# Kernel tuning notes

Hardware: AMD Instinct MI355X
Metric: run time of the kernel (lower is better)

Reference implementation:

```python
import jax, jax.numpy as jnp
import numpy as np

N_POINTS = 8192
N_TOPICS = 64
B = 524288


def setup_inputs() -> dict:
    key = jax.random.key(0)
    k1, k2, k3, k4 = jax.random.split(key, 4)
    pij = jax.random.uniform(k1, (B,), dtype=jnp.float32, minval=1e-6, maxval=1.0)
    i = jax.random.randint(k2, (B,), 0, N_POINTS, dtype=jnp.int64)
    j = jax.random.randint(k3, (B,), 0, N_POINTS, dtype=jnp.int64)
    W = jax.random.normal(k4, (N_POINTS, N_TOPICS), dtype=jnp.float32)  # nn.Embedding weight
    return {"pij": pij, "i": i, "j": j, "W": W}


def reference(pij, i, j, W):
    # pairwise squared distances over ALL points, via the gram trick
    # (avoids materializing the [n, n, d] broadcasted tensor of the torch code)
    sq = jnp.sum(W * W, axis=1)                       # [n]
    d2 = sq[:, None] + sq[None, :] - 2.0 * (W @ W.T)  # [n, n]
    d2 = jnp.maximum(d2, 0.0)                         # numerical floor (exact math is >= 0)
    n = W.shape[0]
    # Cauchy kernel partition: sum_{k,l} 1/(1+d2) minus the n diagonal ones
    part = jnp.sum(1.0 / (1.0 + d2)) - jnp.asarray(n, d2.dtype)
    xi = W[i]                                         # [B, d]
    xj = W[j]                                         # [B, d]
    # FAITHFUL to source: (1 + diff^2).sum(1) adds 1 per dim => n_topics + ||xi-xj||^2
    num = 1.0 / jnp.sum(1.0 + (xi - xj) ** 2, axis=1)  # [B]
    qij = num / part
    loss_kld = pij * (jnp.log(pij) - jnp.log(qij))
    return jnp.sum(loss_kld)
```

## Files before the change

### kernel.cpp

```cpp
#include <hip/hip_runtime.h>
#include <math.h>

#define NPOINTS   8192
#define NDIM      64
#define TILE      128
#define NT2       64
#define NBLK      2080
#define NGRP      512

#define WS_W16   0
#define WS_W8    262144
#define WS_SQ    393216
#define WS_PARTA 401408
#define WS_A1P   403488
#define WS_A3P   407584

typedef __attribute__((ext_vector_type(8))) short bf16x8;
typedef __attribute__((ext_vector_type(4))) float f32x4;
typedef __attribute__((ext_vector_type(2))) float f32x2;

__device__ inline unsigned f2bf_pk(float lo, float hi) {
    unsigned ul = __float_as_uint(lo), uh = __float_as_uint(hi);
    ul += 0x7FFFu + ((ul >> 16) & 1u);
    uh += 0x7FFFu + ((uh >> 16) & 1u);
    return (ul >> 16) | (uh & 0xFFFF0000u);
}
template <bool HI>
__device__ inline f32x2 cvt2(unsigned dw) {
    return __builtin_amdgcn_cvt_pk_f32_fp8((int)dw, HI);
}
__device__ inline void sqacc(f32x2& s, unsigned a, unsigned b) {
    f32x2 dl = cvt2<false>(a) - cvt2<false>(b);
    f32x2 dh = cvt2<true >(a) - cvt2<true >(b);
    s += dl * dl;
    s += dh * dh;
}

__global__ __launch_bounds__(256) void prep_kernel(const float* __restrict__ W,
                                                   float* __restrict__ sq,
                                                   unsigned* __restrict__ W16f,
                                                   unsigned* __restrict__ W8) {
    int g = blockIdx.x;
    int t = threadIdx.x;

    {
        int h = t >> 7, L = (t >> 1) & 63, dp = t & 1;
        int row = g * 16 + (L & 15), quad = L >> 4;
        float4 v = *(const float4*)(W + row * NDIM + h * 32 + quad * 8 + dp * 4);
        uint2 o;
        o.x = f2bf_pk(v.x, v.y);
        o.y = f2bf_pk(v.z, v.w);
        *(uint2*)(W16f + ((g * 2 + h) * 256 + L * 4 + dp * 2)) = o;
    }
    {
        int r = t >> 4, s = t & 15;
        float4 v = *(const float4*)(W + (g * 16 + r) * NDIM + s * 4);
        float p = v.x * v.x + v.y * v.y + v.z * v.z + v.w * v.w;
        p += __shfl_xor(p, 1, 64);
        p += __shfl_xor(p, 2, 64);
        p += __shfl_xor(p, 4, 64);
        p += __shfl_xor(p, 8, 64);
        if (s == 0) sq[g * 16 + r] = p;
    }
    {
        int r = g * 16 + (t >> 4), d = t & 15;
        float4 x = *(const float4*)(W + r * NDIM + d * 4);
        int lo = __builtin_amdgcn_cvt_pk_fp8_f32(x.x, x.y, 0, false);
        int dw = __builtin_amdgcn_cvt_pk_fp8_f32(x.z, x.w, lo, true);
        W8[r * 16 + d] = (unsigned)dw;
    }
}

__global__ __launch_bounds__(256) void pair_kernel(const unsigned* __restrict__ W8,
                                                   const float* __restrict__ pij,
                                                   const int* __restrict__ ii,
                                                   const int* __restrict__ jj,
                                                   int nb,
                                                   float* __restrict__ a1p,
                                                   float* __restrict__ a3p) {
    int t = threadIdx.x;
    int p = blockIdx.x * 256 + t;
    float a1 = 0.f, a3 = 0.f;
    if (p < nb) {
        int   i  = ii[p];
        int   j  = jj[p];
        float pv = pij[p];
        const uint4* X = (const uint4*)(W8 + i * 16);
        const uint4* Y = (const uint4*)(W8 + j * 16);
        uint4 x0 = X[0], x1 = X[1], x2 = X[2], x3 = X[3];
        uint4 y0 = Y[0], y1 = Y[1], y2 = Y[2], y3 = Y[3];
        f32x2 s2 = {0.f, 0.f};
        sqacc(s2, x0.x, y0.x); sqacc(s2, x0.y, y0.y);
        sqacc(s2, x0.z, y0.z); sqacc(s2, x0.w, y0.w);
        sqacc(s2, x1.x, y1.x); sqacc(s2, x1.y, y1.y);
        sqacc(s2, x1.z, y1.z); sqacc(s2, x1.w, y1.w);
        sqacc(s2, x2.x, y2.x); sqacc(s2, x2.y, y2.y);
        sqacc(s2, x2.z, y2.z); sqacc(s2, x2.w, y2.w);
        sqacc(s2, x3.x, y3.x); sqacc(s2, x3.y, y3.y);
        sqacc(s2, x3.z, y3.z); sqacc(s2, x3.w, y3.w);
        float v = s2.x + s2.y;
        a1 = pv * __logf(pv * ((float)NDIM + v));
        a3 = pv;
    }
    #pragma unroll
    for (int m = 32; m >= 1; m >>= 1) {
        a1 += __shfl_xor(a1, m, 64);
        a3 += __shfl_xor(a3, m, 64);
    }
    __shared__ float red[8];
    if ((t & 63) == 0) { red[t >> 6] = a1; red[4 + (t >> 6)] = a3; }
    __syncthreads();
    if (t == 0) {
        a1p[blockIdx.x] = red[0] + red[1] + red[2] + red[3];
        a3p[blockIdx.x] = red[4] + red[5] + red[6] + red[7];
    }
}

__global__ __launch_bounds__(256) void pairwise_kernel(const unsigned* __restrict__ W16f,
                                                       const float* __restrict__ sq,
                                                       float* __restrict__ partA) {
    int z = blockIdx.x;
    int t = threadIdx.x, w = t >> 6, lane = t & 63;
    int by = (int)((129.0f - sqrtf((float)(16641 - 8 * z))) * 0.5f);
    while (by * NT2 - by * (by - 1) / 2 > z) --by;
    while ((by + 1) * NT2 - (by + 1) * by / 2 <= z) ++by;
    int bx = by + (z - (by * NT2 - by * (by - 1) / 2));

    int wm = w >> 1, wn = w & 1, quad = lane >> 4, l15 = lane & 15;
    int a0 = by * TILE, b0 = bx * TILE;

    float4 base1[4];
    float  sqb[4];
    {
        int arow = a0 + wm * 64 + quad * 4;
        #pragma unroll
        for (int tm = 0; tm < 4; ++tm) {
            float4 v = *(const float4*)(sq + arow + tm * 16);
            base1[tm] = (float4){1.0f + v.x, 1.0f + v.y, 1.0f + v.z, 1.0f + v.w};
        }
        int bcol = b0 + wn * 64 + l15;
        #pragma unroll
        for (int tn = 0; tn < 4; ++tn) sqb[tn] = sq[bcol + tn * 16];
    }

    f32x4 acc[4][4];
    #pragma unroll
    for (int i = 0; i < 4; ++i)
        #pragma unroll
        for (int j = 0; j < 4; ++j) acc[i][j] = (f32x4){0.f, 0.f, 0.f, 0.f};

    int gA = (a0 >> 4) + wm * 4;
    int gB = (b0 >> 4) + wn * 4;
    #pragma unroll
    for (int h = 0; h < 2; ++h) {
        bf16x8 af[4], bfr[4];
        #pragma unroll
        for (int tm = 0; tm < 4; ++tm)
            af[tm] = *(const bf16x8*)(W16f + (((gA + tm) * 2 + h) * 256 + lane * 4));
        #pragma unroll
        for (int tn = 0; tn < 4; ++tn)
            bfr[tn] = *(const bf16x8*)(W16f + (((gB + tn) * 2 + h) * 256 + lane * 4));
        #pragma unroll
        for (int tm = 0; tm < 4; ++tm)
            #pragma unroll
            for (int tn = 0; tn < 4; ++tn)
                acc[tm][tn] = __builtin_amdgcn_mfma_f32_16x16x32_bf16(af[tm], bfr[tn],
                                                                      acc[tm][tn], 0, 0, 0);
    }

    float ssum = 0.f;
    if (bx > by) {
        #pragma unroll
        for (int tn = 0; tn < 4; ++tn) {
            float c0 = sqb[tn];
            #pragma unroll
            for (int tm = 0; tm < 4; ++tm) {
                ssum += __builtin_amdgcn_rcpf(fmaf(acc[tm][tn][0], -2.0f, base1[tm].x + c0));
                ssum += __builtin_amdgcn_rcpf(fmaf(acc[tm][tn][1], -2.0f, base1[tm].y + c0));
                ssum += __builtin_amdgcn_rcpf(fmaf(acc[tm][tn][2], -2.0f, base1[tm].z + c0));
                ssum += __builtin_amdgcn_rcpf(fmaf(acc[tm][tn][3], -2.0f, base1[tm].w + c0));
            }
        }
    } else {
        int quad4 = quad * 4;
        #pragma unroll
        for (int tn = 0; tn < 4; ++tn) {
            int cl = wn * 64 + tn * 16 + l15;
            float c0 = sqb[tn];
            float b4[4];
            #pragma unroll
            for (int tm = 0; tm < 4; ++tm) {
                b4[0] = base1[tm].x; b4[1] = base1[tm].y;
                b4[2] = base1[tm].z; b4[3] = base1[tm].w;
                #pragma unroll
                for (int r = 0; r < 4; ++r) {
                    int rl = wm * 64 + tm * 16 + quad4 + r;
                    float inv = __builtin_amdgcn_rcpf(fmaf(acc[tm][tn][r], -2.0f, b4[r] + c0));
                    ssum += (cl > rl) ? inv : 0.f;
                }
            }
        }
    }
    #pragma unroll
    for (int m = 32; m >= 1; m >>= 1) ssum += __shfl_xor(ssum, m, 64);
    __shared__ float wsum[4];
    if (lane == 0) wsum[w] = ssum;
    __syncthreads();
    if (t == 0) partA[z] = wsum[0] + wsum[1] + wsum[2] + wsum[3];
}

__global__ __launch_bounds__(256) void final_kernel(const float* __restrict__ partA,
                                                    const float* __restrict__ a1p,
                                                    const float* __restrict__ a3p,
                                                    int npb,
                                                    float* __restrict__ out) {
    __shared__ double r1[256], r2[256], r3[256];
    int t = threadIdx.x;
    double dpart = 0.0, d1 = 0.0, d3 = 0.0;
    for (int k = t; k < NBLK; k += 256) dpart += (double)partA[k];
    for (int k = t; k < npb; k += 256) { d1 += (double)a1p[k]; d3 += (double)a3p[k]; }
    r1[t] = dpart; r2[t] = d1; r3[t] = d3;
    __syncthreads();
    for (int s = 128; s >= 1; s >>= 1) {
        if (t < s) { r1[t] += r1[t + s]; r2[t] += r2[t + s]; r3[t] += r3[t + s]; }
        __syncthreads();
    }
    if (t == 0) {
        double part = 2.0 * r1[0];
        out[0] = (float)(r2[0] + r3[0] * log(part));
    }
}

extern "C" void kernel_launch(void* const* d_in, const int* in_sizes, int n_in,
                              void* d_out, int out_size, void* d_ws, size_t ws_size,
                              hipStream_t stream) {
    const float* pij = (const float*)d_in[0];
    const int*   ii  = (const int*)d_in[1];
    const int*   jj  = (const int*)d_in[2];
    const float* W   = (const float*)d_in[3];
    float* out = (float*)d_out;
    float* ws  = (float*)d_ws;

    unsigned* W16f  = (unsigned*)ws + WS_W16;
    unsigned* W8    = (unsigned*)ws + WS_W8;
    float*    sqv   = ws + WS_SQ;
    float*    partA = ws + WS_PARTA;
    float*    a1p   = ws + WS_A1P;
    float*    a3p   = ws + WS_A3P;

    int nb  = in_sizes[0];
    int npb = (nb + 255) / 256;

    prep_kernel<<<NGRP, 256, 0, stream>>>(W, sqv, W16f, W8);
    pair_kernel<<<npb, 256, 0, stream>>>(W8, pij, ii, jj, nb, a1p, a3p);
    pairwise_kernel<<<NBLK, 256, 0, stream>>>(W16f, sqv, partA);
    final_kernel<<<1, 256, 0, stream>>>(partA, a1p, a3p, npb, out);
}
```

Baseline: 91.37 us.

## Merge pair, pairwise and final kernels into one launch with last-block reduction

Fuses the pair-loss kernel, the pairwise Cauchy partition kernel and the final reduction into a single grid, where blocks are split by index between the two workloads. The last block to finish, found with an atomic counter, does the final double-precision reduction. The pair path now uses 4 lanes per pair with 16-byte loads and a shuffle reduction. This removes two kernel launches and lets the two independent stages overlap, at the cost of a threadfence and an atomic per block and 4x more pair blocks.

Result: slower. 285.8 us (+212.8%).

```diff
diff --git a/kernel.cpp b/kernel.cpp
--- a/kernel.cpp
+++ b/kernel.cpp
@@ -13,7 +13,8 @@
 #define WS_SQ    393216
 #define WS_PARTA 401408
 #define WS_A1P   403488
-#define WS_A3P   407584
+#define WS_A3P   411680
+#define WS_CNT   419872
 
 typedef __attribute__((ext_vector_type(8))) short bf16x8;
 typedef __attribute__((ext_vector_type(4))) float f32x4;
@@ -39,9 +40,11 @@
 __global__ __launch_bounds__(256) void prep_kernel(const float* __restrict__ W,
                                                    float* __restrict__ sq,
                                                    unsigned* __restrict__ W16f,
-                                                   unsigned* __restrict__ W8) {
+                                                   unsigned* __restrict__ W8,
+                                                   unsigned* __restrict__ cnt) {
     int g = blockIdx.x;
     int t = threadIdx.x;
+    if (g == 0 && t == 0) *cnt = 0u;
 
     {
         int h = t >> 7, L = (t >> 1) & 63, dp = t & 1;
@@ -71,163 +74,172 @@
     }
 }
 
-__global__ __launch_bounds__(256) void pair_kernel(const unsigned* __restrict__ W8,
+__global__ __launch_bounds__(256) void main_kernel(const unsigned* __restrict__ W16f,
+                                                   const unsigned* __restrict__ W8,
+                                                   const float* __restrict__ sq,
                                                    const float* __restrict__ pij,
                                                    const int* __restrict__ ii,
                                                    const int* __restrict__ jj,
                                                    int nb,
+                                                   float* __restrict__ partA,
                                                    float* __restrict__ a1p,
-                                                   float* __restrict__ a3p) {
-    int t = threadIdx.x;
-    int p = blockIdx.x * 256 + t;
-    float a1 = 0.f, a3 = 0.f;
-    if (p < nb) {
-        int   i  = ii[p];
-        int   j  = jj[p];
-        float pv = pij[p];
-        const uint4* X = (const uint4*)(W8 + i * 16);
-        const uint4* Y = (const uint4*)(W8 + j * 16);
-        uint4 x0 = X[0], x1 = X[1], x2 = X[2], x3 = X[3];
-        uint4 y0 = Y[0], y1 = Y[1], y2 = Y[2], y3 = Y[3];
-        f32x2 s2 = {0.f, 0.f};
-        sqacc(s2, x0.x, y0.x); sqacc(s2, x0.y, y0.y);
-        sqacc(s2, x0.z, y0.z); sqacc(s2, x0.w, y0.w);
-        sqacc(s2, x1.x, y1.x); sqacc(s2, x1.y, y1.y);
-        sqacc(s2, x1.z, y1.z); sqacc(s2, x1.w, y1.w);
-        sqacc(s2, x2.x, y2.x); sqacc(s2, x2.y, y2.y);
-        sqacc(s2, x2.z, y2.z); sqacc(s2, x2.w, y2.w);
-        sqacc(s2, x3.x, y3.x); sqacc(s2, x3.y, y3.y);
-        sqacc(s2, x3.z, y3.z); sqacc(s2, x3.w, y3.w);
-        float v = s2.x + s2.y;
-        a1 = pv * __logf(pv * ((float)NDIM + v));
-        a3 = pv;
-    }
-    #pragma unroll
-    for (int m = 32; m >= 1; m >>= 1) {
-        a1 += __shfl_xor(a1, m, 64);
-        a3 += __shfl_xor(a3, m, 64);
-    }
+                                                   float* __restrict__ a3p,
+                                                   unsigned* __restrict__ cnt,
+                                                   float* __restrict__ out) {
     __shared__ float red[8];
-    if ((t & 63) == 0) { red[t >> 6] = a1; red[4 + (t >> 6)] = a3; }
-    __syncthreads();
-    if (t == 0) {
-        a1p[blockIdx.x] = red[0] + red[1] + red[2] + red[3];
-        a3p[blockIdx.x] = red[4] + red[5] + red[6] + red[7];
-    }
-}
-
-__global__ __launch_bounds__(256) void pairwise_kernel(const unsigned* __restrict__ W16f,
-                                                       const float* __restrict__ sq,
-                                                       float* __restrict__ partA) {
-    int z = blockIdx.x;
+    __shared__ bool  lastflag;
+    int zb = blockIdx.x;
     int t = threadIdx.x, w = t >> 6, lane = t & 63;
-    int by = (int)((129.0f - sqrtf((float)(16641 - 8 * z))) * 0.5f);
-    while (by * NT2 - by * (by - 1) / 2 > z) --by;
-    while ((by + 1) * NT2 - (by + 1) * by / 2 <= z) ++by;
-    int bx = by + (z - (by * NT2 - by * (by - 1) / 2));
-
-    int wm = w >> 1, wn = w & 1, quad = lane >> 4, l15 = lane & 15;
-    int a0 = by * TILE, b0 = bx * TILE;
-
-    float4 base1[4];
-    float  sqb[4];
-    {
-        int arow = a0 + wm * 64 + quad * 4;
-        #pragma unroll
-        for (int tm = 0; tm < 4; ++tm) {
-            float4 v = *(const float4*)(sq + arow + tm * 16);
-            base1[tm] = (float4){1.0f + v.x, 1.0f + v.y, 1.0f + v.z, 1.0f + v.w};
-        }
-        int bcol = b0 + wn * 64 + l15;
-        #pragma unroll
-        for (int tn = 0; tn < 4; ++tn) sqb[tn] = sq[bcol + tn * 16];
-    }
-
-    f32x4 acc[4][4];
-    #pragma unroll
-    for (int i = 0; i < 4; ++i)
-        #pragma unroll
-        for (int j = 0; j < 4; ++j) acc[i][j] = (f32x4){0.f, 0.f, 0.f, 0.f};
-
-    int gA = (a0 >> 4) + wm * 4;
-    int gB = (b0 >> 4) + wn * 4;
-    #pragma unroll
-    for (int h = 0; h < 2; ++h) {
-        bf16x8 af[4], bfr[4];
-        #pragma unroll
-        for (int tm = 0; tm < 4; ++tm)
-            af[tm] = *(const bf16x8*)(W16f + (((gA + tm) * 2 + h) * 256 + lane * 4));
-        #pragma unroll
-        for (int tn = 0; tn < 4; ++tn)
-            bfr[tn] = *(const bf16x8*)(W16f + (((gB + tn) * 2 + h) * 256 + lane * 4));
-        #pragma unroll
-        for (int tm = 0; tm < 4; ++tm)
+
+    if (zb < NBLK) {
+        int z = zb;
+        int by = (int)((129.0f - sqrtf((float)(16641 - 8 * z))) * 0.5f);
+        while (by * NT2 - by * (by - 1) / 2 > z) --by;
+        while ((by + 1) * NT2 - (by + 1) * by / 2 <= z) ++by;
+        int bx = by + (z - (by * NT2 - by * (by - 1) / 2));
+
+        int wm = w >> 1, wn = w & 1, quad = lane >> 4, l15 = lane & 15;
+        int a0 = by * TILE, b0 = bx * TILE;
+
+        float4 base1[4];
+        float  sqb[4];
+        {
+            int arow = a0 + wm * 64 + quad * 4;
+            #pragma unroll
+            for (int tm = 0; tm < 4; ++tm) {
+                float4 v = *(const float4*)(sq + arow + tm * 16);
+                base1[tm] = (float4){1.0f + v.x, 1.0f + v.y, 1.0f + v.z, 1.0f + v.w};
+            }
+            int bcol = b0 + wn * 64 + l15;
+            #pragma unroll
+            for (int tn = 0; tn < 4; ++tn) sqb[tn] = sq[bcol + tn * 16];
+        }
+
+        f32x4 acc[4][4];
+        #pragma unroll
+        for (int i = 0; i < 4; ++i)
+            #pragma unroll
+            for (int j = 0; j < 4; ++j) acc[i][j] = (f32x4){0.f, 0.f, 0.f, 0.f};
+
+        int gA = (a0 >> 4) + wm * 4;
+        int gB = (b0 >> 4) + wn * 4;
+        #pragma unroll
+        for (int h = 0; h < 2; ++h) {
+            bf16x8 af[4], bfr[4];
+            #pragma unroll
+            for (int tm = 0; tm < 4; ++tm)
+                af[tm] = *(const bf16x8*)(W16f + (((gA + tm) * 2 + h) * 256 + lane * 4));
             #pragma unroll
             for (int tn = 0; tn < 4; ++tn)
-                acc[tm][tn] = __builtin_amdgcn_mfma_f32_16x16x32_bf16(af[tm], bfr[tn],
-                                                                      acc[tm][tn], 0, 0, 0);
-    }
-
-    float ssum = 0.f;
-    if (bx > by) {
-        #pragma unroll
-        for (int tn = 0; tn < 4; ++tn) {
-            float c0 = sqb[tn];
-            #pragma unroll
-            for (int tm = 0; tm < 4; ++tm) {
-                ssum += __builtin_amdgcn_rcpf(fmaf(acc[tm][tn][0], -2.0f, base1[tm].x + c0));
-                ssum += __builtin_amdgcn_rcpf(fmaf(acc[tm][tn][1], -2.0f, base1[tm].y + c0));
-                ssum += __builtin_amdgcn_rcpf(fmaf(acc[tm][tn][2], -2.0f, base1[tm].z + c0));
-                ssum += __builtin_amdgcn_rcpf(fmaf(acc[tm][tn][3], -2.0f, base1[tm].w + c0));
-            }
-        }
-    } else {
-        int quad4 = quad * 4;
-        #pragma unroll
-        for (int tn = 0; tn < 4; ++tn) {
-            int cl = wn * 64 + tn * 16 + l15;
-            float c0 = sqb[tn];
-            float b4[4];
-            #pragma unroll
-            for (int tm = 0; tm < 4; ++tm) {
-                b4[0] = base1[tm].x; b4[1] = base1[tm].y;
-                b4[2] = base1[tm].z; b4[3] = base1[tm].w;
+                bfr[tn] = *(const bf16x8*)(W16f + (((gB + tn) * 2 + h) * 256 + lane * 4));
+            #pragma unroll
+            for (int tm = 0; tm < 4; ++tm)
                 #pragma unroll
-                for (int r = 0; r < 4; ++r) {
-                    int rl = wm * 64 + tm * 16 + quad4 + r;
-                    float inv = __builtin_amdgcn_rcpf(fmaf(acc[tm][tn][r], -2.0f, b4[r] + c0));
-                    ssum += (cl > rl) ? inv : 0.f;
+                for (int tn = 0; tn < 4; ++tn)
+                    acc[tm][tn] = __builtin_amdgcn_mfma_f32_16x16x32_bf16(af[tm], bfr[tn],
+                                                                          acc[tm][tn], 0, 0, 0);
+        }
+
+        float ssum = 0.f;
+        if (bx > by) {
+            #pragma unroll
+            for (int tn = 0; tn < 4; ++tn) {
+                float c0 = sqb[tn];
+                #pragma unroll
+                for (int tm = 0; tm < 4; ++tm) {
+                    ssum += __builtin_amdgcn_rcpf(fmaf(acc[tm][tn][0], -2.0f, base1[tm].x + c0));
+                    ssum += __builtin_amdgcn_rcpf(fmaf(acc[tm][tn][1], -2.0f, base1[tm].y + c0));
+                    ssum += __builtin_amdgcn_rcpf(fmaf(acc[tm][tn][2], -2.0f, base1[tm].z + c0));
+                    ssum += __builtin_amdgcn_rcpf(fmaf(acc[tm][tn][3], -2.0f, base1[tm].w + c0));
                 }
             }
-        }
-    }
-    #pragma unroll
-    for (int m = 32; m >= 1; m >>= 1) ssum += __shfl_xor(ssum, m, 64);
-    __shared__ float wsum[4];
-    if (lane == 0) wsum[w] = ssum;
+        } else {
+            int quad4 = quad * 4;
+            #pragma unroll
+            for (int tn = 0; tn < 4; ++tn) {
+                int cl = wn * 64 + tn * 16 + l15;
+                float c0 = sqb[tn];
+                float b4[4];
+                #pragma unroll
+                for (int tm = 0; tm < 4; ++tm) {
+                    b4[0] = base1[tm].x; b4[1] = base1[tm].y;
+                    b4[2] = base1[tm].z; b4[3] = base1[tm].w;
+                    #pragma unroll
+                    for (int r = 0; r < 4; ++r) {
+                        int rl = wm * 64 + tm * 16 + quad4 + r;
+                        float inv = __builtin_amdgcn_rcpf(fmaf(acc[tm][tn][r], -2.0f, b4[r] + c0));
+                        ssum += (cl > rl) ? inv : 0.f;
+                    }
+                }
+            }
+        }
+        #pragma unroll
+        for (int m = 32; m >= 1; m >>= 1) ssum += __shfl_xor(ssum, m, 64);
+        if (lane == 0) red[w] = ssum;
+        __syncthreads();
+        if (t == 0) partA[z] = red[0] + red[1] + red[2] + red[3];
+    } else {
+        int pb = zb - NBLK;
+        int g  = lane >> 2;
+        int s  = lane & 3;
+        int p  = pb * 64 + w * 16 + g;
+        float a1 = 0.f, a3 = 0.f;
+        if (p < nb) {
+            int   i  = ii[p];
+            int   j  = jj[p];
+            float pv = pij[p];
+            uint4 xi = *(const uint4*)(W8 + i * 16 + s * 4);
+            uint4 xj = *(const uint4*)(W8 + j * 16 + s * 4);
+            f32x2 s2 = {0.f, 0.f};
+            sqacc(s2, xi.x, xj.x);
+            sqacc(s2, xi.y, xj.y);
+            sqacc(s2, xi.z, xj.z);
+            sqacc(s2, xi.w, xj.w);
+            float v = s2.x + s2.y;
+            v += __shfl_xor(v, 1, 64);
+            v += __shfl_xor(v, 2, 64);
+            a1 = pv * __logf(pv * ((float)NDIM + v));
+            a3 = pv;
+        }
+        #pragma unroll
+        for (int m = 32; m >= 1; m >>= 1) {
+            a1 += __shfl_xor(a1, m, 64);
+            a3 += __shfl_xor(a3, m, 64);
+        }
+        if (lane == 0) { red[w] = a1 * 0.25f; red[4 + w] = a3 * 0.25f; }
+        __syncthreads();
+        if (t == 0) {
+            a1p[pb] = red[0] + red[1] + red[2] + red[3];
+            a3p[pb] = red[4] + red[5] + red[6] + red[7];
+        }
+    }
+
+    if (t == 0) {
+        __threadfence();
+        unsigned old = atomicAdd(cnt, 1u);
+        lastflag = (old == gridDim.x - 1);
+    }
     __syncthreads();
-    if (t == 0) partA[z] = wsum[0] + wsum[1] + wsum[2] + wsum[3];
-}
-
-__global__ __launch_bounds__(256) void final_kernel(const float* __restrict__ partA,
-                                                    const float* __restrict__ a1p,
-                                                    const float* __restrict__ a3p,
-                                                    int npb,
-                                                    float* __restrict__ out) {
-    __shared__ double r1[256], r2[256], r3[256];
-    int t = threadIdx.x;
+    if (!lastflag) return;
+
+    __shared__ double r1s[256], r2s[256], r3s[256];
+    int npb = (int)gridDim.x - NBLK;
     double dpart = 0.0, d1 = 0.0, d3 = 0.0;
-    for (int k = t; k < NBLK; k += 256) dpart += (double)partA[k];
-    for (int k = t; k < npb; k += 256) { d1 += (double)a1p[k]; d3 += (double)a3p[k]; }
-    r1[t] = dpart; r2[t] = d1; r3[t] = d3;
+    for (int k = t; k < NBLK; k += 256)
+        dpart += (double)__hip_atomic_load(&partA[k], __ATOMIC_RELAXED, __HIP_MEMORY_SCOPE_AGENT);
+    for (int k = t; k < npb; k += 256) {
+        d1 += (double)__hip_atomic_load(&a1p[k], __ATOMIC_RELAXED, __HIP_MEMORY_SCOPE_AGENT);
+        d3 += (double)__hip_atomic_load(&a3p[k], __ATOMIC_RELAXED, __HIP_MEMORY_SCOPE_AGENT);
+    }
+    r1s[t] = dpart; r2s[t] = d1; r3s[t] = d3;
     __syncthreads();
-    for (int s = 128; s >= 1; s >>= 1) {
-        if (t < s) { r1[t] += r1[t + s]; r2[t] += r2[t + s]; r3[t] += r3[t + s]; }
+    for (int s2 = 128; s2 >= 1; s2 >>= 1) {
+        if (t < s2) { r1s[t] += r1s[t + s2]; r2s[t] += r2s[t + s2]; r3s[t] += r3s[t + s2]; }
         __syncthreads();
     }
     if (t == 0) {
-        double part = 2.0 * r1[0];
-        out[0] = (float)(r2[0] + r3[0] * log(part));
+        double part = 2.0 * r1s[0];
+        out[0] = (float)(r2s[0] + r3s[0] * log(part));
     }
 }
 
@@ -247,12 +259,12 @@
     float*    partA = ws + WS_PARTA;
     float*    a1p   = ws + WS_A1P;
     float*    a3p   = ws + WS_A3P;
+    unsigned* cnt   = (unsigned*)ws + WS_CNT;
 
     int nb  = in_sizes[0];
-    int npb = (nb + 255) / 256;
-
-    prep_kernel<<<NGRP, 256, 0, stream>>>(W, sqv, W16f, W8);
-    pair_kernel<<<npb, 256, 0, stream>>>(W8, pij, ii, jj, nb, a1p, a3p);
-    pairwise_kernel<<<NBLK, 256, 0, stream>>>(W16f, sqv, partA);
-    final_kernel<<<1, 256, 0, stream>>>(partA, a1p, a3p, npb, out);
-}
+    int npb = (nb + 63) / 64;
+
+    prep_kernel<<<NGRP, 256, 0, stream>>>(W, sqv, W16f, W8, cnt);
+    main_kernel<<<NBLK + npb, 256, 0, stream>>>(W16f, W8, sqv, pij, ii, jj, nb,
+                                                partA, a1p, a3p, cnt, out);
+}
```
